# Performance work log

Hardware: AMD Instinct MI355X
Metric: run time of the kernel (lower is better)

## Reference

```python
import jax, jax.numpy as jnp
import numpy as np

N, E, F_IN = 50000, 250000, 128
H1, H2, HEADS = 64, 32, 4
D1 = H1 * HEADS   # 256 = conv1 output dim (concat)
D2 = H2 * HEADS   # 128 = conv2 output dim (concat)
EPS_BN = 1e-5


def setup_inputs() -> dict:
    key = jax.random.key(0)
    ks = iter(jax.random.split(key, 64))
    def nrm(shape, scale=0.05):
        return jax.random.normal(next(ks), shape, dtype=jnp.float32) * scale
    inp = {}
    inp['x'] = jax.random.normal(next(ks), (N, F_IN), dtype=jnp.float32)
    inp['edge_index'] = jax.random.randint(next(ks), (2, E), 0, N, dtype=jnp.int32)
    inp['neg_edge_index'] = jax.random.randint(next(ks), (2, E), 0, N, dtype=jnp.int32)
    # conv1: TransformerConv(F_IN, 64, heads=4, beta=True, concat=True)
    inp['Wq1'] = nrm((F_IN, D1)); inp['bq1'] = jnp.zeros((D1,), jnp.float32)
    inp['Wk1'] = nrm((F_IN, D1)); inp['bk1'] = jnp.zeros((D1,), jnp.float32)
    inp['Wv1'] = nrm((F_IN, D1)); inp['bv1'] = jnp.zeros((D1,), jnp.float32)
    inp['Ws1'] = nrm((F_IN, D1)); inp['bs1'] = jnp.zeros((D1,), jnp.float32)
    inp['Wb1'] = nrm((3 * D1, 1))
    inp['g1'] = jnp.ones((D1,), jnp.float32); inp['be1'] = jnp.zeros((D1,), jnp.float32)
    inp['m1'] = nrm((D1,), 0.01); inp['v1'] = jax.random.uniform(next(ks), (D1,), dtype=jnp.float32) + 0.5
    # conv2: TransformerConv(256, 32, heads=4, beta=True, concat=True)
    inp['Wq2'] = nrm((D1, D2)); inp['bq2'] = jnp.zeros((D2,), jnp.float32)
    inp['Wk2'] = nrm((D1, D2)); inp['bk2'] = jnp.zeros((D2,), jnp.float32)
    inp['Wv2'] = nrm((D1, D2)); inp['bv2'] = jnp.zeros((D2,), jnp.float32)
    inp['Ws2'] = nrm((D1, D2)); inp['bs2'] = jnp.zeros((D2,), jnp.float32)
    inp['Wb2'] = nrm((3 * D2, 1))
    inp['g2'] = jnp.ones((D2,), jnp.float32); inp['be2'] = jnp.zeros((D2,), jnp.float32)
    inp['m2'] = nrm((D2,), 0.01); inp['v2'] = jax.random.uniform(next(ks), (D2,), dtype=jnp.float32) + 0.5
    # conv3: TransformerConv(128, 1, heads=1, beta=True, concat=False)
    inp['Wq3'] = nrm((D2, 1)); inp['bq3'] = jnp.zeros((1,), jnp.float32)
    inp['Wk3'] = nrm((D2, 1)); inp['bk3'] = jnp.zeros((1,), jnp.float32)
    inp['Wv3'] = nrm((D2, 1)); inp['bv3'] = jnp.zeros((1,), jnp.float32)
    inp['Ws3'] = nrm((D2, 1)); inp['bs3'] = jnp.zeros((1,), jnp.float32)
    inp['Wb3'] = nrm((3, 1))
    inp['c1'] = jnp.float32(0.5); inp['c2'] = jnp.float32(0.5)
    return inp


def _tconv(h, src, dst, Wq, bq, Wk, bk, Wv, bv, Ws, bs, Wb, heads, dh):
    # PyG TransformerConv with beta=True, root_weight=True. Messages flow src -> dst.
    n = h.shape[0]
    q = (h @ Wq + bq).reshape(n, heads, dh)
    k = (h @ Wk + bk).reshape(n, heads, dh)
    v = (h @ Wv + bv).reshape(n, heads, dh)
    score = jnp.einsum('ehd,ehd->eh', q[dst], k[src]) / jnp.sqrt(jnp.float32(dh))  # [E,H]
    m = jax.ops.segment_max(score, dst, num_segments=n)
    m = jnp.where(jnp.isfinite(m), m, jnp.float32(0.0))  # empty segments
    p = jnp.exp(score - m[dst])
    denom = jax.ops.segment_sum(p, dst, num_segments=n)
    alpha = p / (denom[dst] + 1e-16)
    out = jax.ops.segment_sum(alpha[:, :, None] * v[src], dst, num_segments=n)  # [N,H,dh]
    out = out.reshape(n, heads * dh)  # concat (heads=1 for conv3 -> same as mean)
    x_r = h @ Ws + bs
    beta = jax.nn.sigmoid(jnp.concatenate([out, x_r, out - x_r], axis=-1) @ Wb)  # [N,1]
    return beta * x_r + (1.0 - beta) * out


def _bn_eval(x, g, b, m, v):
    return (x - m) * jax.lax.rsqrt(v + EPS_BN) * g + b


def reference(x, edge_index, neg_edge_index,
              Wq1, bq1, Wk1, bk1, Wv1, bv1, Ws1, bs1, Wb1, g1, be1, m1, v1,
              Wq2, bq2, Wk2, bk2, Wv2, bv2, Ws2, bs2, Wb2, g2, be2, m2, v2,
              Wq3, bq3, Wk3, bk3, Wv3, bv3, Ws3, bs3, Wb3, c1, c2):
    src, dst = edge_index[0], edge_index[1]
    h = _tconv(x, src, dst, Wq1, bq1, Wk1, bk1, Wv1, bv1, Ws1, bs1, Wb1, HEADS, H1)
    h = jax.nn.elu(_bn_eval(h, g1, be1, m1, v1))
    h = _tconv(h, src, dst, Wq2, bq2, Wk2, bk2, Wv2, bv2, Ws2, bs2, Wb2, HEADS, H2)
    z = jax.nn.elu(_bn_eval(h, g2, be2, m2, v2))
    pos = -jnp.log(jax.nn.sigmoid(jnp.sum(z[src] * z[dst], axis=1)) + 1e-15).mean()
    ns, nd = neg_edge_index[0], neg_edge_index[1]
    neg = -jnp.log(1.0 - jax.nn.sigmoid(jnp.sum(z[ns] * z[nd], axis=1)) + 1e-15).mean()
    r_loss = pos + neg
    x_out = _tconv(z, src, dst, Wq3, bq3, Wk3, bk3, Wv3, bv3, Ws3, bs3, Wb3, 1, 1)
    return (x_out, r_loss, c1, c2)
```

## Files before the change

kernel.cpp:

```cpp
#include <hip/hip_runtime.h>
#include <hip/hip_bf16.h>

typedef _Float16 half8 __attribute__((ext_vector_type(8)));
typedef _Float16 half4 __attribute__((ext_vector_type(4)));
typedef _Float16 half2v __attribute__((ext_vector_type(2)));
typedef float f32x4 __attribute__((ext_vector_type(4)));

__global__ __launch_bounds__(256) void prep_w(
    const float* __restrict__ W0, const float* __restrict__ W1,
    const float* __restrict__ W2, const float* __restrict__ W3,
    _Float16* __restrict__ T, int K, int D)
{
  int idx = blockIdx.x * 256 + threadIdx.x;
  int tot = K * D;
  if (idx >= 4 * tot) return;
  int which = idx / tot, rem = idx - which * tot;
  int d = rem / K, k = rem - d * K;
  const float* W = which == 0 ? W0 : which == 1 ? W1 : which == 2 ? W2 : W3;
  T[idx] = (_Float16)W[(long long)k * D + d];
}

template<int K, typename OutT>
__global__ __launch_bounds__(256) void mfma_gemm(
    const float* __restrict__ A, const _Float16* __restrict__ Wt,
    const float* __restrict__ bias, OutT* __restrict__ C, int Nr, int Dout)
{
  int lane = threadIdx.x & 63;
  int w    = threadIdx.x >> 6;
  int wm = w >> 1, wn = w & 1;
  int row0 = blockIdx.x * 64 + wm * 32;
  int col0 = blockIdx.y * 64 + wn * 32;
  int lr = lane & 15;
  int lk = (lane >> 4) * 8;

  f32x4 acc[2][2] = {};
#pragma unroll
  for (int kb = 0; kb < K; kb += 32) {
    half8 a[2], b[2];
#pragma unroll
    for (int mt = 0; mt < 2; ++mt) {
      int row = row0 + mt * 16 + lr;
      if (row < Nr) {
        const float* p = A + (long long)row * K + kb + lk;
        float4 f0 = *(const float4*)p;
        float4 f1 = *(const float4*)(p + 4);
        a[mt][0] = (_Float16)f0.x; a[mt][1] = (_Float16)f0.y;
        a[mt][2] = (_Float16)f0.z; a[mt][3] = (_Float16)f0.w;
        a[mt][4] = (_Float16)f1.x; a[mt][5] = (_Float16)f1.y;
        a[mt][6] = (_Float16)f1.z; a[mt][7] = (_Float16)f1.w;
      } else {
        a[mt] = half8{};
      }
    }
#pragma unroll
    for (int nt = 0; nt < 2; ++nt) {
      int col = col0 + nt * 16 + lr;
      b[nt] = *(const half8*)(Wt + (long long)col * K + kb + lk);
    }
#pragma unroll
    for (int mt = 0; mt < 2; ++mt)
#pragma unroll
      for (int nt = 0; nt < 2; ++nt)
        acc[mt][nt] = __builtin_amdgcn_mfma_f32_16x16x32_f16(a[mt], b[nt], acc[mt][nt], 0, 0, 0);
  }
#pragma unroll
  for (int nt = 0; nt < 2; ++nt) {
    int col = col0 + nt * 16 + lr;
    float bc = bias[col];
#pragma unroll
    for (int mt = 0; mt < 2; ++mt) {
      int r0 = row0 + mt * 16 + (lane >> 4) * 4;
#pragma unroll
      for (int i = 0; i < 4; ++i) {
        int row = r0 + i;
        if (row < Nr) C[(long long)row * Dout + col] = (OutT)(acc[mt][nt][i] + bc);
      }
    }
  }
}

__global__ __launch_bounds__(256) void csr_hist(
    const int* __restrict__ ei, int E, int* __restrict__ cnt)
{
  int e = blockIdx.x * 256 + threadIdx.x;
  if (e >= E) return;
  atomicAdd(&cnt[ei[E + e]], 1);
}

__global__ __launch_bounds__(256) void csr_scan1(
    const int* __restrict__ cnt, int* __restrict__ excl,
    int* __restrict__ chunkSums, int N)
{
  int b = blockIdx.x, t = threadIdx.x;
  int lane = t & 63, w = t >> 6;
  int base = b * 1024 + t * 4;
  int c[4];
#pragma unroll
  for (int j = 0; j < 4; ++j) c[j] = (base + j < N) ? cnt[base + j] : 0;
  int ts = c[0] + c[1] + c[2] + c[3];
  int s = ts;
#pragma unroll
  for (int d = 1; d < 64; d <<= 1) {
    int u = __shfl_up(s, d, 64);
    if (lane >= d) s += u;
  }
  __shared__ int wsum[4];
  if (lane == 63) wsum[w] = s;
  __syncthreads();
  int woff = 0;
  for (int i = 0; i < w; ++i) woff += wsum[i];
  int off = woff + s - ts;
#pragma unroll
  for (int j = 0; j < 4; ++j) {
    if (base + j < N) excl[base + j] = off;
    off += c[j];
  }
  if (t == 0) chunkSums[b] = wsum[0] + wsum[1] + wsum[2] + wsum[3];
}

__global__ void csr_scan2(int* __restrict__ chunkSums, int nch,
                          int* __restrict__ rowptr, int N, int E)
{
  int lane = threadIdx.x;
  int v = (lane < nch) ? chunkSums[lane] : 0;
  int s = v;
#pragma unroll
  for (int d = 1; d < 64; d <<= 1) {
    int u = __shfl_up(s, d, 64);
    if (lane >= d) s += u;
  }
  if (lane < nch) chunkSums[lane] = s - v;
  if (lane == 0) rowptr[N] = E;
}

__global__ __launch_bounds__(256) void csr_scan3(
    int* __restrict__ rowptr, const int* __restrict__ chunkSums, int N)
{
  int i = blockIdx.x * 256 + threadIdx.x;
  if (i < N) rowptr[i] += chunkSums[i >> 10];
}

__global__ __launch_bounds__(256) void csr_scatter(
    const int* __restrict__ ei, int E, const int* __restrict__ rowptr,
    int* __restrict__ fill, int* __restrict__ csr_src)
{
  int e = blockIdx.x * 256 + threadIdx.x;
  if (e >= E) return;
  int s = ei[e], d = ei[E + e];
  int pos = atomicAdd(&fill[d], 1);
  csr_src[rowptr[d] + pos] = s;
}

template<int D, int H>
__global__ __launch_bounds__(256) void attn_fused(
    const int* __restrict__ rowptr, const int* __restrict__ csr_src,
    const float* __restrict__ q, const _Float16* __restrict__ k,
    const _Float16* __restrict__ v, float* __restrict__ o, int N)
{
  constexpr int PER = D / 64;
  constexpr int DH  = D / H;
  int node = blockIdx.x * 4 + (threadIdx.x >> 6);
  if (node >= N) return;
  int lane = threadIdx.x & 63;
  int j0   = lane * PER;
  const float inv = 1.0f / sqrtf((float)DH);

  float qv[PER];
  if constexpr (PER == 4) {
    float4 t4 = *(const float4*)(q + (long long)node * D + j0);
    qv[0]=t4.x; qv[1]=t4.y; qv[2]=t4.z; qv[3]=t4.w;
  } else {
    float2 t2 = *(const float2*)(q + (long long)node * D + j0);
    qv[0]=t2.x; qv[1]=t2.y;
  }

  float m = -INFINITY, den = 0.f;
  float acc[PER] = {};
  int beg = rowptr[node], end = rowptr[node + 1];
  for (int i = beg; i < end; ++i) {
    int s = csr_src[i];
    float kv[PER], vv[PER];
    if constexpr (PER == 4) {
      half4 t4 = *(const half4*)(k + (long long)s * D + j0);
      half4 u4 = *(const half4*)(v + (long long)s * D + j0);
#pragma unroll
      for (int j = 0; j < 4; ++j) { kv[j] = (float)t4[j]; vv[j] = (float)u4[j]; }
    } else {
      half2v t2 = *(const half2v*)(k + (long long)s * D + j0);
      half2v u2 = *(const half2v*)(v + (long long)s * D + j0);
#pragma unroll
      for (int j = 0; j < 2; ++j) { kv[j] = (float)t2[j]; vv[j] = (float)u2[j]; }
    }
    float dot = 0.f;
#pragma unroll
    for (int j = 0; j < PER; ++j) dot += qv[j] * kv[j];
    dot += __shfl_xor(dot, 8, 64);
    dot += __shfl_xor(dot, 4, 64);
    dot += __shfl_xor(dot, 2, 64);
    dot += __shfl_xor(dot, 1, 64);
    float score = dot * inv;
    float nm = fmaxf(m, score);
    float scale = __expf(m - nm);
    float p = __expf(score - nm);
    den = den * scale + p;
#pragma unroll
    for (int j = 0; j < PER; ++j) acc[j] = acc[j] * scale + p * vv[j];
    m = nm;
  }
  float r = 1.f / (den + 1e-16f);
  if constexpr (PER == 4) {
    float4 w4; w4.x = acc[0]*r; w4.y = acc[1]*r; w4.z = acc[2]*r; w4.w = acc[3]*r;
    *(float4*)(o + (long long)node * D + j0) = w4;
  } else {
    float2 w2; w2.x = acc[0]*r; w2.y = acc[1]*r;
    *(float2*)(o + (long long)node * D + j0) = w2;
  }
}

template<int D, bool WRITE_H>
__global__ __launch_bounds__(256) void node_gate2(
    const float* __restrict__ o, const float* __restrict__ xr,
    const float* __restrict__ Wb, const float* __restrict__ g,
    const float* __restrict__ be, const float* __restrict__ bm,
    const float* __restrict__ bv, float* __restrict__ out,
    _Float16* __restrict__ outh, int N)
{
  constexpr int PER = D / 64;
  int node = blockIdx.x * 4 + (threadIdx.x >> 6);
  if (node >= N) return;
  int lane = threadIdx.x & 63;
  int j0   = lane * PER;
  float ov[PER], xv[PER];
  if constexpr (PER == 4) {
    float4 o4 = *(const float4*)(o  + (long long)node * D + j0);
    float4 x4 = *(const float4*)(xr + (long long)node * D + j0);
    ov[0]=o4.x; ov[1]=o4.y; ov[2]=o4.z; ov[3]=o4.w;
    xv[0]=x4.x; xv[1]=x4.y; xv[2]=x4.z; xv[3]=x4.w;
  } else {
    float2 o2 = *(const float2*)(o  + (long long)node * D + j0);
    float2 x2 = *(const float2*)(xr + (long long)node * D + j0);
    ov[0]=o2.x; ov[1]=o2.y;
    xv[0]=x2.x; xv[1]=x2.y;
  }
  float dot = 0.f;
#pragma unroll
  for (int i = 0; i < PER; ++i) {
    int j = j0 + i;
    dot += ov[i] * Wb[j] + xv[i] * Wb[D + j] + (ov[i] - xv[i]) * Wb[2 * D + j];
  }
#pragma unroll
  for (int off = 32; off >= 1; off >>= 1) dot += __shfl_xor(dot, off, 64);
  float beta = 1.f / (1.f + expf(-dot));
  float res[PER];
#pragma unroll
  for (int i = 0; i < PER; ++i) {
    int j = j0 + i;
    float h = beta * xv[i] + (1.f - beta) * ov[i];
    float y = (h - bm[j]) * rsqrtf(bv[j] + 1e-5f) * g[j] + be[j];
    res[i] = y > 0.f ? y : expf(y) - 1.f;
  }
  if constexpr (PER == 4) {
    float4 w; w.x=res[0]; w.y=res[1]; w.z=res[2]; w.w=res[3];
    *(float4*)(out + (long long)node * D + j0) = w;
  } else {
    float2 w; w.x=res[0]; w.y=res[1];
    *(float2*)(out + (long long)node * D + j0) = w;
  }
  if constexpr (WRITE_H) {
    if constexpr (PER == 4) {
      half4 hw; hw[0]=(_Float16)res[0]; hw[1]=(_Float16)res[1];
      hw[2]=(_Float16)res[2]; hw[3]=(_Float16)res[3];
      *(half4*)(outh + (long long)node * D + j0) = hw;
    } else {
      half2v hw; hw[0]=(_Float16)res[0]; hw[1]=(_Float16)res[1];
      *(half2v*)(outh + (long long)node * D + j0) = hw;
    }
  }
}

__global__ __launch_bounds__(256) void loss_kernel(
    const int* __restrict__ ei, const int* __restrict__ nei,
    const _Float16* __restrict__ zh, int E, float* __restrict__ acc)
{
  int lane = threadIdx.x & 63;
  int wib  = threadIdx.x >> 6;
  int sub  = lane >> 5, r = lane & 31;
  long long gw = ((long long)blockIdx.x * blockDim.x + threadIdx.x) >> 6;
  long long nw = ((long long)gridDim.x * blockDim.x) >> 6;
  float lpos = 0.f, lneg = 0.f;
  for (long long w = gw * 2 + sub; w < 2LL * E; w += nw * 2) {
    int isneg = (w >= E);
    const int* ep = isneg ? nei : ei;
    long long idx = isneg ? w - E : w;
    int s = ep[idx], d = ep[E + idx];
    half4 a = *(const half4*)(zh + (long long)s * 128 + r * 4);
    half4 b = *(const half4*)(zh + (long long)d * 128 + r * 4);
    float dot = (float)a[0]*(float)b[0] + (float)a[1]*(float)b[1]
              + (float)a[2]*(float)b[2] + (float)a[3]*(float)b[3];
#pragma unroll
    for (int off = 16; off >= 1; off >>= 1) dot += __shfl_xor(dot, off, 64);
    if (r == 0) {
      float sg = 1.f / (1.f + expf(-dot));
      if (isneg) lneg += -logf(1.f - sg + 1e-15f);
      else       lpos += -logf(sg + 1e-15f);
    }
  }
#pragma unroll
  for (int off = 32; off >= 1; off >>= 1) {
    lpos += __shfl_xor(lpos, off, 64);
    lneg += __shfl_xor(lneg, off, 64);
  }
  __shared__ float sp[4], sn[4];
  if (lane == 0) { sp[wib] = lpos; sn[wib] = lneg; }
  __syncthreads();
  if (threadIdx.x == 0) {
    float P = 0.f, Ng = 0.f;
    for (int i = 0; i < 4; ++i) { P += sp[i]; Ng += sn[i]; }
    atomicAdd(acc, P);
    atomicAdd(acc + 1, Ng);
  }
}

__global__ __launch_bounds__(256) void gemv4(
    const float* __restrict__ z,
    const float* __restrict__ Wq, const float* __restrict__ bq,
    const float* __restrict__ Wk, const float* __restrict__ bk,
    const float* __restrict__ Wv, const float* __restrict__ bv,
    const float* __restrict__ Ws, const float* __restrict__ bs,
    float* __restrict__ q3, float* __restrict__ k3,
    float* __restrict__ v3, float* __restrict__ s3, int N)
{
  int node = blockIdx.x * 4 + (threadIdx.x >> 6);
  if (node >= N) return;
  int lane = threadIdx.x & 63;
  float2 zv = *(const float2*)(z + (long long)node * 128 + lane * 2);
  float aq = zv.x * Wq[lane*2] + zv.y * Wq[lane*2+1];
  float ak = zv.x * Wk[lane*2] + zv.y * Wk[lane*2+1];
  float av = zv.x * Wv[lane*2] + zv.y * Wv[lane*2+1];
  float as_ = zv.x * Ws[lane*2] + zv.y * Ws[lane*2+1];
#pragma unroll
  for (int off = 32; off >= 1; off >>= 1) {
    aq  += __shfl_xor(aq,  off, 64);
    ak  += __shfl_xor(ak,  off, 64);
    av  += __shfl_xor(av,  off, 64);
    as_ += __shfl_xor(as_, off, 64);
  }
  if (lane == 0) {
    q3[node] = aq + bq[0];
    k3[node] = ak + bk[0];
    v3[node] = av + bv[0];
    s3[node] = as_ + bs[0];
  }
}

__global__ __launch_bounds__(256) void attn3_node(
    const int* __restrict__ rowptr, const int* __restrict__ csr_src,
    const float* __restrict__ q3, const float* __restrict__ k3,
    const float* __restrict__ v3, const float* __restrict__ s3,
    const float* __restrict__ Wb3, float* __restrict__ out, int N)
{
  int n = blockIdx.x * 256 + threadIdx.x;
  if (n >= N) return;
  float qd = q3[n];
  float m = -INFINITY, den = 0.f, acc = 0.f;
  int beg = rowptr[n], end = rowptr[n + 1];
  for (int i = beg; i < end; ++i) {
    int s = csr_src[i];
    float sc = qd * k3[s];
    float nm = fmaxf(m, sc);
    float scale = __expf(m - nm);
    float p = __expf(sc - nm);
    den = den * scale + p;
    acc = acc * scale + p * v3[s];
    m = nm;
  }
  float on = acc / (den + 1e-16f);
  float xr = s3[n];
  float tv = on * Wb3[0] + xr * Wb3[1] + (on - xr) * Wb3[2];
  float b = 1.f / (1.f + expf(-tv));
  out[n] = b * xr + (1.f - b) * on;
}

__global__ void finalize_kernel(const float* __restrict__ acc,
                                const float* __restrict__ c1, const float* __restrict__ c2,
                                float* __restrict__ out, int N, int E)
{
  out[N]     = acc[0] / (float)E + acc[1] / (float)E;
  out[N + 1] = c1[0];
  out[N + 2] = c2[0];
}

extern "C" void kernel_launch(void* const* d_in, const int* in_sizes, int n_in,
                              void* d_out, int out_size, void* d_ws, size_t ws_size,
                              hipStream_t stream)
{
  const float* x   = (const float*)d_in[0];
  const int*   ei  = (const int*)d_in[1];
  const int*   nei = (const int*)d_in[2];
  const float* Wq1 = (const float*)d_in[3];  const float* bq1 = (const float*)d_in[4];
  const float* Wk1 = (const float*)d_in[5];  const float* bk1 = (const float*)d_in[6];
  const float* Wv1 = (const float*)d_in[7];  const float* bv1 = (const float*)d_in[8];
  const float* Ws1 = (const float*)d_in[9];  const float* bs1 = (const float*)d_in[10];
  const float* Wb1 = (const float*)d_in[11];
  const float* g1  = (const float*)d_in[12]; const float* be1 = (const float*)d_in[13];
  const float* m1  = (const float*)d_in[14]; const float* v1  = (const float*)d_in[15];
  const float* Wq2 = (const float*)d_in[16]; const float* bq2 = (const float*)d_in[17];
  const float* Wk2 = (const float*)d_in[18]; const float* bk2 = (const float*)d_in[19];
  const float* Wv2 = (const float*)d_in[20]; const float* bv2 = (const float*)d_in[21];
  const float* Ws2 = (const float*)d_in[22]; const float* bs2 = (const float*)d_in[23];
  const float* Wb2 = (const float*)d_in[24];
  const float* g2  = (const float*)d_in[25]; const float* be2 = (const float*)d_in[26];
  const float* m2  = (const float*)d_in[27]; const float* v2  = (const float*)d_in[28];
  const float* Wq3 = (const float*)d_in[29]; const float* bq3 = (const float*)d_in[30];
  const float* Wk3 = (const float*)d_in[31]; const float* bk3 = (const float*)d_in[32];
  const float* Wv3 = (const float*)d_in[33]; const float* bv3 = (const float*)d_in[34];
  const float* Ws3 = (const float*)d_in[35]; const float* bs3 = (const float*)d_in[36];
  const float* Wb3 = (const float*)d_in[37];
  const float* c1  = (const float*)d_in[38]; const float* c2  = (const float*)d_in[39];

  const int N = in_sizes[0] / 128;
  const int E = in_sizes[1] / 2;

  float* ws = (float*)d_ws;
  float* B0 = ws;
  float* B1 = B0 + (size_t)N * 256;
  float* B2 = B1 + (size_t)N * 256;
  int* rowptr = (int*)(B2 + (size_t)N * 256);
  int* cnt    = rowptr + (N + 1);
  int* csrs   = cnt + N;
  int* chks   = csrs + E;
  float* accbuf = (float*)(chks + 64);
  uintptr_t wp = ((uintptr_t)(accbuf + 2) + 63) & ~(uintptr_t)63;
  _Float16* wt1 = (_Float16*)wp;
  _Float16* wt2 = wt1 + 4 * 32768;

  size_t need = ((size_t)3 * N * 256) * 4 + ((size_t)2 * N + 1 + E + 64) * 4 + 8
              + 64 + 8 * 32768 * sizeof(_Float16);
  if (ws_size < need) return;

  float* out = (float*)d_out;
  dim3 blk(256);
  int ng  = (N + 3) / 4;
  int egE = (E + 255) / 256;
  int egN = (N + 255) / 256;
  int nch = (N + 1023) / 1024;
  dim3 g1grid((N + 63) / 64, 256 / 64);
  dim3 g2grid((N + 63) / 64, 128 / 64);

  prep_w<<<(4 * 32768 + 255) / 256, blk, 0, stream>>>(Wq1, Wk1, Wv1, Ws1, wt1, 128, 256);
  prep_w<<<(4 * 32768 + 255) / 256, blk, 0, stream>>>(Wq2, Wk2, Wv2, Ws2, wt2, 256, 128);

  (void)hipMemsetAsync(cnt, 0, (size_t)N * sizeof(int), stream);
  csr_hist<<<egE, blk, 0, stream>>>(ei, E, cnt);
  csr_scan1<<<nch, blk, 0, stream>>>(cnt, rowptr, chks, N);
  csr_scan2<<<1, 64, 0, stream>>>(chks, nch, rowptr, N, E);
  csr_scan3<<<egN, blk, 0, stream>>>(rowptr, chks, N);
  (void)hipMemsetAsync(cnt, 0, (size_t)N * sizeof(int), stream);
  csr_scatter<<<egE, blk, 0, stream>>>(ei, E, rowptr, cnt, csrs);

  _Float16* k1h = (_Float16*)B1;
  _Float16* v1h = (_Float16*)B2;
  mfma_gemm<128, float>   <<<g1grid, blk, 0, stream>>>(x, wt1 + 0 * 32768, bq1, B0,  N, 256);
  mfma_gemm<128, _Float16><<<g1grid, blk, 0, stream>>>(x, wt1 + 1 * 32768, bk1, k1h, N, 256);
  mfma_gemm<128, _Float16><<<g1grid, blk, 0, stream>>>(x, wt1 + 2 * 32768, bv1, v1h, N, 256);
  attn_fused<256,4><<<ng, blk, 0, stream>>>(rowptr, csrs, B0, k1h, v1h, B0, N);
  mfma_gemm<128, float>   <<<g1grid, blk, 0, stream>>>(x, wt1 + 3 * 32768, bs1, B1, N, 256);
  node_gate2<256,false><<<ng, blk, 0, stream>>>(B0, B1, Wb1, g1, be1, m1, v1, B2, nullptr, N);

  float*    q2p = B0;
  _Float16* k2h = (_Float16*)(B0 + (size_t)N * 128);
  _Float16* v2h = (_Float16*)B1;
  float*    s2p = B1 + (size_t)N * 128;
  mfma_gemm<256, float>   <<<g2grid, blk, 0, stream>>>(B2, wt2 + 0 * 32768, bq2, q2p, N, 128);
  mfma_gemm<256, _Float16><<<g2grid, blk, 0, stream>>>(B2, wt2 + 1 * 32768, bk2, k2h, N, 128);
  mfma_gemm<256, _Float16><<<g2grid, blk, 0, stream>>>(B2, wt2 + 2 * 32768, bv2, v2h, N, 128);
  attn_fused<128,4><<<ng, blk, 0, stream>>>(rowptr, csrs, q2p, k2h, v2h, q2p, N);
  mfma_gemm<256, float>   <<<g2grid, blk, 0, stream>>>(B2, wt2 + 3 * 32768, bs2, s2p, N, 128);
  float*    z  = B0 + (size_t)N * 128;
  _Float16* zh = (_Float16*)B2;
  node_gate2<128,true><<<ng, blk, 0, stream>>>(q2p, s2p, Wb2, g2, be2, m2, v2, z, zh, N);

  (void)hipMemsetAsync(accbuf, 0, 2 * sizeof(float), stream);
  loss_kernel<<<2048, blk, 0, stream>>>(ei, nei, zh, E, accbuf);

  float* q3 = B1;
  float* k3 = B1 + (size_t)N;
  float* v3 = B1 + (size_t)2 * N;
  float* s3 = B1 + (size_t)3 * N;
  gemv4<<<ng, blk, 0, stream>>>(z, Wq3, bq3, Wk3, bk3, Wv3, bv3, Ws3, bs3, q3, k3, v3, s3, N);
  attn3_node<<<egN, blk, 0, stream>>>(rowptr, csrs, q3, k3, v3, s3, Wb3, out, N);

  finalize_kernel<<<1, 1, 0, stream>>>(accbuf, c1, c2, out, N, E);
}
```

Before: 798.8 us.

## Fuse Q/K/V/skip projections into one GEMM launch per layer and widen loss loads

The four separate projection GEMMs per conv layer are merged into one launch over the concatenated fp16 weight matrix. Each 64-column tile picks its output segment, bias and output dtype from its column index. Buffers are reassigned so the skip projection is computed alongside Q/K/V, which frees space for the later stages. The loss kernel now uses 16 lanes per edge with 8-wide half loads, handling four edges per wavefront instead of two, which cuts shuffle-reduction steps.

```diff
diff --git a/kernel.cpp b/kernel.cpp
--- a/kernel.cpp
+++ b/kernel.cpp
@@ -20,16 +20,22 @@
   T[idx] = (_Float16)W[(long long)k * D + d];
 }
 
-template<int K, typename OutT>
-__global__ __launch_bounds__(256) void mfma_gemm(
-    const float* __restrict__ A, const _Float16* __restrict__ Wt,
-    const float* __restrict__ bias, OutT* __restrict__ C, int Nr, int Dout)
+template<int K, int SEGW>
+__global__ __launch_bounds__(256) void fused_gemm(
+    const float* __restrict__ A, const _Float16* __restrict__ Wcat,
+    const float* __restrict__ b0, const float* __restrict__ b1,
+    const float* __restrict__ b2, const float* __restrict__ b3,
+    float* __restrict__ o0, _Float16* __restrict__ o1,
+    _Float16* __restrict__ o2, float* __restrict__ o3, int Nr)
 {
   int lane = threadIdx.x & 63;
   int w    = threadIdx.x >> 6;
   int wm = w >> 1, wn = w & 1;
-  int row0 = blockIdx.x * 64 + wm * 32;
-  int col0 = blockIdx.y * 64 + wn * 32;
+  int row0  = blockIdx.x * 64 + wm * 32;
+  int gcol0 = blockIdx.y * 64 + wn * 32;
+  int seg   = (blockIdx.y * 64) / SEGW;
+  int lcol0 = blockIdx.y * 64 - seg * SEGW + wn * 32;
+  const float* bias = seg == 0 ? b0 : seg == 1 ? b1 : seg == 2 ? b2 : b3;
   int lr = lane & 15;
   int lk = (lane >> 4) * 8;
 
@@ -54,8 +60,8 @@
     }
 #pragma unroll
     for (int nt = 0; nt < 2; ++nt) {
-      int col = col0 + nt * 16 + lr;
-      b[nt] = *(const half8*)(Wt + (long long)col * K + kb + lk);
+      int gc = gcol0 + nt * 16 + lr;
+      b[nt] = *(const half8*)(Wcat + (long long)gc * K + kb + lk);
     }
 #pragma unroll
     for (int mt = 0; mt < 2; ++mt)
@@ -65,15 +71,22 @@
   }
 #pragma unroll
   for (int nt = 0; nt < 2; ++nt) {
-    int col = col0 + nt * 16 + lr;
-    float bc = bias[col];
+    int lcol = lcol0 + nt * 16 + lr;
+    float bc = bias[lcol];
 #pragma unroll
     for (int mt = 0; mt < 2; ++mt) {
       int r0 = row0 + mt * 16 + (lane >> 4) * 4;
 #pragma unroll
       for (int i = 0; i < 4; ++i) {
         int row = r0 + i;
-        if (row < Nr) C[(long long)row * Dout + col] = (OutT)(acc[mt][nt][i] + bc);
+        if (row < Nr) {
+          float val = acc[mt][nt][i] + bc;
+          long long off = (long long)row * SEGW + lcol;
+          if      (seg == 0) o0[off] = val;
+          else if (seg == 1) o1[off] = (_Float16)val;
+          else if (seg == 2) o2[off] = (_Float16)val;
+          else               o3[off] = val;
+        }
       }
     }
   }
@@ -284,32 +297,36 @@
 {
   int lane = threadIdx.x & 63;
   int wib  = threadIdx.x >> 6;
-  int sub  = lane >> 5, r = lane & 31;
+  int sub  = lane >> 4;
+  int r    = lane & 15;
   long long gw = ((long long)blockIdx.x * blockDim.x + threadIdx.x) >> 6;
   long long nw = ((long long)gridDim.x * blockDim.x) >> 6;
   float lpos = 0.f, lneg = 0.f;
-  for (long long w = gw * 2 + sub; w < 2LL * E; w += nw * 2) {
-    int isneg = (w >= E);
-    const int* ep = isneg ? nei : ei;
-    long long idx = isneg ? w - E : w;
-    int s = ep[idx], d = ep[E + idx];
-    half4 a = *(const half4*)(zh + (long long)s * 128 + r * 4);
-    half4 b = *(const half4*)(zh + (long long)d * 128 + r * 4);
-    float dot = (float)a[0]*(float)b[0] + (float)a[1]*(float)b[1]
-              + (float)a[2]*(float)b[2] + (float)a[3]*(float)b[3];
-#pragma unroll
-    for (int off = 16; off >= 1; off >>= 1) dot += __shfl_xor(dot, off, 64);
-    if (r == 0) {
-      float sg = 1.f / (1.f + expf(-dot));
-      if (isneg) lneg += -logf(1.f - sg + 1e-15f);
-      else       lpos += -logf(sg + 1e-15f);
+  for (long long base = gw * 4; base < 2LL * E; base += nw * 4) {
+    long long wq = base + sub;
+    if (wq < 2LL * E) {
+      int isneg = (wq >= E);
+      const int* ep = isneg ? nei : ei;
+      long long idx = isneg ? wq - E : wq;
+      int s = ep[idx], d = ep[E + idx];
+      half8 a = *(const half8*)(zh + (long long)s * 128 + r * 8);
+      half8 b = *(const half8*)(zh + (long long)d * 128 + r * 8);
+      float dot = 0.f;
+#pragma unroll
+      for (int j = 0; j < 8; ++j) dot += (float)a[j] * (float)b[j];
+      dot += __shfl_xor(dot, 8, 64);
+      dot += __shfl_xor(dot, 4, 64);
+      dot += __shfl_xor(dot, 2, 64);
+      dot += __shfl_xor(dot, 1, 64);
+      if (r == 0) {
+        float sg = 1.f / (1.f + expf(-dot));
+        if (isneg) lneg += -logf(1.f - sg + 1e-15f);
+        else       lpos += -logf(sg + 1e-15f);
+      }
     }
   }
-#pragma unroll
-  for (int off = 32; off >= 1; off >>= 1) {
-    lpos += __shfl_xor(lpos, off, 64);
-    lneg += __shfl_xor(lneg, off, 64);
-  }
+  lpos += __shfl_xor(lpos, 16, 64); lpos += __shfl_xor(lpos, 32, 64);
+  lneg += __shfl_xor(lneg, 16, 64); lneg += __shfl_xor(lneg, 32, 64);
   __shared__ float sp[4], sn[4];
   if (lane == 0) { sp[wib] = lpos; sn[wib] = lneg; }
   __syncthreads();
@@ -444,8 +461,8 @@
   int egE = (E + 255) / 256;
   int egN = (N + 255) / 256;
   int nch = (N + 1023) / 1024;
-  dim3 g1grid((N + 63) / 64, 256 / 64);
-  dim3 g2grid((N + 63) / 64, 128 / 64);
+  dim3 fg1((N + 63) / 64, 1024 / 64);
+  dim3 fg2((N + 63) / 64, 512 / 64);
 
   prep_w<<<(4 * 32768 + 255) / 256, blk, 0, stream>>>(Wq1, Wk1, Wv1, Ws1, wt1, 128, 256);
   prep_w<<<(4 * 32768 + 255) / 256, blk, 0, stream>>>(Wq2, Wk2, Wv2, Ws2, wt2, 256, 128);
@@ -459,34 +476,30 @@
   csr_scatter<<<egE, blk, 0, stream>>>(ei, E, rowptr, cnt, csrs);
 
   _Float16* k1h = (_Float16*)B1;
-  _Float16* v1h = (_Float16*)B2;
-  mfma_gemm<128, float>   <<<g1grid, blk, 0, stream>>>(x, wt1 + 0 * 32768, bq1, B0,  N, 256);
-  mfma_gemm<128, _Float16><<<g1grid, blk, 0, stream>>>(x, wt1 + 1 * 32768, bk1, k1h, N, 256);
-  mfma_gemm<128, _Float16><<<g1grid, blk, 0, stream>>>(x, wt1 + 2 * 32768, bv1, v1h, N, 256);
+  _Float16* v1h = k1h + (size_t)N * 256;
+  fused_gemm<128,256><<<fg1, blk, 0, stream>>>(x, wt1, bq1, bk1, bv1, bs1,
+                                               B0, k1h, v1h, B2, N);
   attn_fused<256,4><<<ng, blk, 0, stream>>>(rowptr, csrs, B0, k1h, v1h, B0, N);
-  mfma_gemm<128, float>   <<<g1grid, blk, 0, stream>>>(x, wt1 + 3 * 32768, bs1, B1, N, 256);
-  node_gate2<256,false><<<ng, blk, 0, stream>>>(B0, B1, Wb1, g1, be1, m1, v1, B2, nullptr, N);
+  node_gate2<256,false><<<ng, blk, 0, stream>>>(B0, B2, Wb1, g1, be1, m1, v1, B1, nullptr, N);
 
   float*    q2p = B0;
   _Float16* k2h = (_Float16*)(B0 + (size_t)N * 128);
-  _Float16* v2h = (_Float16*)B1;
-  float*    s2p = B1 + (size_t)N * 128;
-  mfma_gemm<256, float>   <<<g2grid, blk, 0, stream>>>(B2, wt2 + 0 * 32768, bq2, q2p, N, 128);
-  mfma_gemm<256, _Float16><<<g2grid, blk, 0, stream>>>(B2, wt2 + 1 * 32768, bk2, k2h, N, 128);
-  mfma_gemm<256, _Float16><<<g2grid, blk, 0, stream>>>(B2, wt2 + 2 * 32768, bv2, v2h, N, 128);
+  _Float16* v2h = k2h + (size_t)N * 128;
+  float*    s2p = B2;
+  fused_gemm<256,128><<<fg2, blk, 0, stream>>>(B1, wt2, bq2, bk2, bv2, bs2,
+                                               q2p, k2h, v2h, s2p, N);
   attn_fused<128,4><<<ng, blk, 0, stream>>>(rowptr, csrs, q2p, k2h, v2h, q2p, N);
-  mfma_gemm<256, float>   <<<g2grid, blk, 0, stream>>>(B2, wt2 + 3 * 32768, bs2, s2p, N, 128);
-  float*    z  = B0 + (size_t)N * 128;
-  _Float16* zh = (_Float16*)B2;
+  float*    z  = B1;
+  _Float16* zh = (_Float16*)(B2 + (size_t)N * 128);
   node_gate2<128,true><<<ng, blk, 0, stream>>>(q2p, s2p, Wb2, g2, be2, m2, v2, z, zh, N);
 
   (void)hipMemsetAsync(accbuf, 0, 2 * sizeof(float), stream);
   loss_kernel<<<2048, blk, 0, stream>>>(ei, nei, zh, E, accbuf);
 
-  float* q3 = B1;
-  float* k3 = B1 + (size_t)N;
-  float* v3 = B1 + (size_t)2 * N;
-  float* s3 = B1 + (size_t)3 * N;
+  float* q3 = B2;
+  float* k3 = B2 + (size_t)N;
+  float* v3 = B2 + (size_t)2 * N;
+  float* s3 = B2 + (size_t)3 * N;
   gemv4<<<ng, blk, 0, stream>>>(z, Wq3, bq3, Wk3, bk3, Wv3, bv3, Ws3, bs3, q3, k3, v3, s3, N);
   attn3_node<<<egN, blk, 0, stream>>>(rowptr, csrs, q3, k3, v3, s3, Wb3, out, N);
 
```

Result: faster. 739.8 us (-7.4%).
